# Kernel tuning notes

Measured on AMD Instinct MI355X. Metric: run time of the kernel, lower is better.

Reference implementation:

```python
import jax, jax.numpy as jnp
import numpy as np

N_NODES = 100000
N_EDGES = 1200000
IN_DIM = 64
OUT_DIM = 64


def setup_inputs() -> dict:
    key = jax.random.key(0)
    k1, k2, k3, k4, k5 = jax.random.split(key, 5)
    x = jax.random.normal(k1, (N_NODES, IN_DIM), dtype=jnp.float32)
    src = jax.random.randint(k2, (N_EDGES,), 0, N_NODES, dtype=jnp.int32)
    dst = jax.random.randint(k3, (N_EDGES,), 0, N_NODES, dtype=jnp.int32)
    # nn.Linear(in_dim, out_dim): weight [out, in], bias [out]
    bound = 1.0 / np.sqrt(IN_DIM)
    W = jax.random.uniform(k4, (OUT_DIM, IN_DIM), minval=-bound, maxval=bound, dtype=jnp.float32)
    b = jax.random.uniform(k5, (OUT_DIM,), minval=-bound, maxval=bound, dtype=jnp.float32)
    return {"x": x, "src": src, "dst": dst, "W": W, "b": b}


def reference(x, src, dst, W, b):
    # copy_u('h','m') + mean('m','h_neigh'): per-destination mean of source features
    msg_sum = jax.ops.segment_sum(x[src], dst, num_segments=N_NODES)  # [N, in_dim]
    deg = jax.ops.segment_sum(jnp.ones_like(dst, dtype=x.dtype), dst, num_segments=N_NODES)
    h = msg_sum / jnp.maximum(deg, 1.0)[:, None]  # isolated nodes -> 0 (DGL mean semantics)
    # linear: h @ W^T + b
    return h @ W.T + b
```

## Files before the change

### kernel.cpp

```cpp
#include <hip/hip_runtime.h>

#define N_NODES 100000
#define N_EDGES 1200000
#define DIM 64
#define NPW 8
#define WPB 4


__global__ __launch_bounds__(256) void hist_rank_kernel(
    const int* __restrict__ dst, int* __restrict__ counts,
    int* __restrict__ rank, int n4)
{
    int i = blockIdx.x * blockDim.x + threadIdx.x;
    if (i >= n4) return;
    int4 d = ((const int4*)dst)[i];
    int r0 = atomicAdd(&counts[d.x], 1);
    int r1 = atomicAdd(&counts[d.y], 1);
    int r2 = atomicAdd(&counts[d.z], 1);
    int r3 = atomicAdd(&counts[d.w], 1);
    ((int4*)rank)[i] = make_int4(r0, r1, r2, r3);
}

__global__ __launch_bounds__(256) void offsets_kernel(
    const int* __restrict__ counts, int* __restrict__ offsets,
    int* __restrict__ base_counter, int n)
{
    __shared__ int tmp[256];
    __shared__ int base;
    int i = blockIdx.x * 256 + threadIdx.x;
    int v = (i < n) ? counts[i] : 0;
    tmp[threadIdx.x] = v;
    __syncthreads();
    #pragma unroll
    for (int d = 1; d < 256; d <<= 1) {
        int t = (threadIdx.x >= d) ? tmp[threadIdx.x - d] : 0;
        __syncthreads();
        tmp[threadIdx.x] += t;
        __syncthreads();
    }
    if (threadIdx.x == 255) base = atomicAdd(base_counter, tmp[255]);
    __syncthreads();
    if (i < n) offsets[i] = base + tmp[threadIdx.x] - v;
}

__global__ __launch_bounds__(256) void fill_kernel(
    const int* __restrict__ src, const int* __restrict__ dst,
    const int* __restrict__ rank, const int* __restrict__ offsets,
    int* __restrict__ csr_src, int n4)
{
    int i = blockIdx.x * blockDim.x + threadIdx.x;
    if (i >= n4) return;
    int4 s = ((const int4*)src)[i];
    int4 d = ((const int4*)dst)[i];
    int4 r = ((const int4*)rank)[i];
    csr_src[offsets[d.x] + r.x] = s.x;
    csr_src[offsets[d.y] + r.y] = s.y;
    csr_src[offsets[d.z] + r.z] = s.z;
    csr_src[offsets[d.w] + r.w] = s.w;
}

__global__ __launch_bounds__(256) void aggregate_linear_kernel(
    const float* __restrict__ x, const int* __restrict__ csr_src,
    const int* __restrict__ offsets, const int* __restrict__ counts,
    const float* __restrict__ W, const float* __restrict__ bias,
    float* __restrict__ out, int n_nodes)
{
    __shared__ float Ws[DIM][68];
    __shared__ float hs[WPB][DIM];

    for (int i = threadIdx.x; i < DIM * DIM / 4; i += 256) {
        float4 wv = ((const float4*)W)[i];
        int o = (i * 4) >> 6, f = (i * 4) & 63;
        *(float4*)&Ws[o][f] = wv;
    }
    __syncthreads();

    int w    = threadIdx.x >> 6;
    int lane = threadIdx.x & 63;
    float bl = bias[lane];

    int node0 = (blockIdx.x * WPB + w) * NPW;
    #pragma unroll 1
    for (int ni = 0; ni < NPW; ++ni) {
        int node = node0 + ni;
        if (node >= n_nodes) break;

        int off = offsets[node];
        int deg = counts[node];
        int end = off + deg;
        float a0 = 0.f, a1 = 0.f, a2 = 0.f, a3 = 0.f;
        int k = off;
        for (; k + 3 < end; k += 4) {
            int s0 = csr_src[k];
            int s1 = csr_src[k + 1];
            int s2 = csr_src[k + 2];
            int s3 = csr_src[k + 3];
            a0 += x[(size_t)s0 * DIM + lane];
            a1 += x[(size_t)s1 * DIM + lane];
            a2 += x[(size_t)s2 * DIM + lane];
            a3 += x[(size_t)s3 * DIM + lane];
        }
        for (; k < end; ++k) a0 += x[(size_t)csr_src[k] * DIM + lane];
        float h = ((a0 + a1) + (a2 + a3)) / fmaxf((float)deg, 1.0f);

        hs[w][lane] = h;
        __builtin_amdgcn_wave_barrier();

        float acc = bl;
        #pragma unroll
        for (int f0 = 0; f0 < DIM; f0 += 4) {
            float4 hv = *(const float4*)&hs[w][f0];
            float4 wv = *(const float4*)&Ws[lane][f0];
            acc = fmaf(hv.x, wv.x, acc);
            acc = fmaf(hv.y, wv.y, acc);
            acc = fmaf(hv.z, wv.z, acc);
            acc = fmaf(hv.w, wv.w, acc);
        }
        out[(size_t)node * DIM + lane] = acc;
        __builtin_amdgcn_wave_barrier();
    }
}

extern "C" void kernel_launch(void* const* d_in, const int* in_sizes, int n_in,
                              void* d_out, int out_size, void* d_ws, size_t ws_size,
                              hipStream_t stream) {
    const float* x   = (const float*)d_in[0];
    const int*   src = (const int*)d_in[1];
    const int*   dst = (const int*)d_in[2];
    const float* W   = (const float*)d_in[3];
    const float* b   = (const float*)d_in[4];
    float* out = (float*)d_out;

    int* counts       = (int*)d_ws;
    int* base_counter = counts + 100032;
    int* offsets      = base_counter + 32;
    int* rank         = offsets + 100032;
    int* csr_src      = rank + N_EDGES;

    hipMemsetAsync(counts, 0, (size_t)(100032 + 32) * sizeof(int), stream);

    int n4 = N_EDGES / 4;
    int eb4 = (n4 + 255) / 256;
    int nb = (N_NODES + 255) / 256;

    hist_rank_kernel<<<eb4, 256, 0, stream>>>(dst, counts, rank, n4);
    offsets_kernel  <<<nb, 256, 0, stream>>>(counts, offsets, base_counter, N_NODES);
    fill_kernel     <<<eb4, 256, 0, stream>>>(src, dst, rank, offsets, csr_src, n4);

    int blocks = (N_NODES + WPB * NPW - 1) / (WPB * NPW);
    aggregate_linear_kernel<<<blocks, 256, 0, stream>>>(
        x, csr_src, offsets, counts, W, b, out, N_NODES);
}
```

Measured before the change: 225.2 us.

## Gather neighbor rows as float4 across quarter-waves and widen edge kernels

The aggregation loop now splits each wave into four 16-lane groups, so each group loads a whole neighbor row as float4 and eight edges are processed per iteration. Partial sums are then combined with cross-lane shuffles. The histogram and fill kernels each handle eight edges per thread, and the output store is made nontemporal. This aims to raise memory-level parallelism in the gather and cut per-edge instruction overhead, at the cost of predicated tail loads and extra shuffle reductions for low-degree nodes.

After: 214.2 us. 1.05x faster.

```diff
diff --git a/kernel.cpp b/kernel.cpp
--- a/kernel.cpp
+++ b/kernel.cpp
@@ -9,16 +9,23 @@
 
 __global__ __launch_bounds__(256) void hist_rank_kernel(
     const int* __restrict__ dst, int* __restrict__ counts,
-    int* __restrict__ rank, int n4)
+    int* __restrict__ rank, int n8)
 {
     int i = blockIdx.x * blockDim.x + threadIdx.x;
-    if (i >= n4) return;
-    int4 d = ((const int4*)dst)[i];
-    int r0 = atomicAdd(&counts[d.x], 1);
-    int r1 = atomicAdd(&counts[d.y], 1);
-    int r2 = atomicAdd(&counts[d.z], 1);
-    int r3 = atomicAdd(&counts[d.w], 1);
-    ((int4*)rank)[i] = make_int4(r0, r1, r2, r3);
+    if (i >= n8) return;
+    int4 d0 = ((const int4*)dst)[2 * i];
+    int4 d1 = ((const int4*)dst)[2 * i + 1];
+    int4 r0, r1;
+    r0.x = atomicAdd(&counts[d0.x], 1);
+    r0.y = atomicAdd(&counts[d0.y], 1);
+    r0.z = atomicAdd(&counts[d0.z], 1);
+    r0.w = atomicAdd(&counts[d0.w], 1);
+    r1.x = atomicAdd(&counts[d1.x], 1);
+    r1.y = atomicAdd(&counts[d1.y], 1);
+    r1.z = atomicAdd(&counts[d1.z], 1);
+    r1.w = atomicAdd(&counts[d1.w], 1);
+    ((int4*)rank)[2 * i]     = r0;
+    ((int4*)rank)[2 * i + 1] = r1;
 }
 
 __global__ __launch_bounds__(256) void offsets_kernel(
@@ -46,17 +53,24 @@
 __global__ __launch_bounds__(256) void fill_kernel(
     const int* __restrict__ src, const int* __restrict__ dst,
     const int* __restrict__ rank, const int* __restrict__ offsets,
-    int* __restrict__ csr_src, int n4)
+    int* __restrict__ csr_src, int n8)
 {
     int i = blockIdx.x * blockDim.x + threadIdx.x;
-    if (i >= n4) return;
-    int4 s = ((const int4*)src)[i];
-    int4 d = ((const int4*)dst)[i];
-    int4 r = ((const int4*)rank)[i];
-    csr_src[offsets[d.x] + r.x] = s.x;
-    csr_src[offsets[d.y] + r.y] = s.y;
-    csr_src[offsets[d.z] + r.z] = s.z;
-    csr_src[offsets[d.w] + r.w] = s.w;
+    if (i >= n8) return;
+    int4 s0 = ((const int4*)src)[2 * i];
+    int4 s1 = ((const int4*)src)[2 * i + 1];
+    int4 d0 = ((const int4*)dst)[2 * i];
+    int4 d1 = ((const int4*)dst)[2 * i + 1];
+    int4 r0 = ((const int4*)rank)[2 * i];
+    int4 r1 = ((const int4*)rank)[2 * i + 1];
+    csr_src[offsets[d0.x] + r0.x] = s0.x;
+    csr_src[offsets[d0.y] + r0.y] = s0.y;
+    csr_src[offsets[d0.z] + r0.z] = s0.z;
+    csr_src[offsets[d0.w] + r0.w] = s0.w;
+    csr_src[offsets[d1.x] + r1.x] = s1.x;
+    csr_src[offsets[d1.y] + r1.y] = s1.y;
+    csr_src[offsets[d1.z] + r1.z] = s1.z;
+    csr_src[offsets[d1.w] + r1.w] = s1.w;
 }
 
 __global__ __launch_bounds__(256) void aggregate_linear_kernel(
@@ -70,13 +84,15 @@
 
     for (int i = threadIdx.x; i < DIM * DIM / 4; i += 256) {
         float4 wv = ((const float4*)W)[i];
-        int o = (i * 4) >> 6, f = (i * 4) & 63;
-        *(float4*)&Ws[o][f] = wv;
+        int o = i >> 4, fq = i & 15;
+        *(float4*)&Ws[o][fq * 4] = wv;
     }
     __syncthreads();
 
     int w    = threadIdx.x >> 6;
     int lane = threadIdx.x & 63;
+    int g    = lane >> 4;
+    int gl   = lane & 15;
     float bl = bias[lane];
 
     int node0 = (blockIdx.x * WPB + w) * NPW;
@@ -88,22 +104,31 @@
         int off = offsets[node];
         int deg = counts[node];
         int end = off + deg;
-        float a0 = 0.f, a1 = 0.f, a2 = 0.f, a3 = 0.f;
-        int k = off;
-        for (; k + 3 < end; k += 4) {
-            int s0 = csr_src[k];
-            int s1 = csr_src[k + 1];
-            int s2 = csr_src[k + 2];
-            int s3 = csr_src[k + 3];
-            a0 += x[(size_t)s0 * DIM + lane];
-            a1 += x[(size_t)s1 * DIM + lane];
-            a2 += x[(size_t)s2 * DIM + lane];
-            a3 += x[(size_t)s3 * DIM + lane];
+        float4 a0 = {0.f, 0.f, 0.f, 0.f};
+        float4 a1 = {0.f, 0.f, 0.f, 0.f};
+        for (int k = off; k < end; k += 8) {
+            int e0 = k + g, e1 = k + 4 + g;
+            int s0 = csr_src[min(e0, end - 1)];
+            int s1 = csr_src[min(e1, end - 1)];
+            float4 v0 = *(const float4*)&x[(size_t)s0 * DIM + gl * 4];
+            float4 v1 = *(const float4*)&x[(size_t)s1 * DIM + gl * 4];
+            bool p0 = e0 < end, p1 = e1 < end;
+            a0.x += p0 ? v0.x : 0.f;  a0.y += p0 ? v0.y : 0.f;
+            a0.z += p0 ? v0.z : 0.f;  a0.w += p0 ? v0.w : 0.f;
+            a1.x += p1 ? v1.x : 0.f;  a1.y += p1 ? v1.y : 0.f;
+            a1.z += p1 ? v1.z : 0.f;  a1.w += p1 ? v1.w : 0.f;
         }
-        for (; k < end; ++k) a0 += x[(size_t)csr_src[k] * DIM + lane];
-        float h = ((a0 + a1) + (a2 + a3)) / fmaxf((float)deg, 1.0f);
+        a0.x += a1.x; a0.y += a1.y; a0.z += a1.z; a0.w += a1.w;
+        a0.x += __shfl_xor(a0.x, 16, 64); a0.x += __shfl_xor(a0.x, 32, 64);
+        a0.y += __shfl_xor(a0.y, 16, 64); a0.y += __shfl_xor(a0.y, 32, 64);
+        a0.z += __shfl_xor(a0.z, 16, 64); a0.z += __shfl_xor(a0.z, 32, 64);
+        a0.w += __shfl_xor(a0.w, 16, 64); a0.w += __shfl_xor(a0.w, 32, 64);
 
-        hs[w][lane] = h;
+        float inv = 1.0f / fmaxf((float)deg, 1.0f);
+        if (g == 0) {
+            float4 h4 = {a0.x * inv, a0.y * inv, a0.z * inv, a0.w * inv};
+            *(float4*)&hs[w][gl * 4] = h4;
+        }
         __builtin_amdgcn_wave_barrier();
 
         float acc = bl;
@@ -116,7 +141,7 @@
             acc = fmaf(hv.z, wv.z, acc);
             acc = fmaf(hv.w, wv.w, acc);
         }
-        out[(size_t)node * DIM + lane] = acc;
+        __builtin_nontemporal_store(acc, &out[(size_t)node * DIM + lane]);
         __builtin_amdgcn_wave_barrier();
     }
 }
@@ -139,13 +164,13 @@
 
     hipMemsetAsync(counts, 0, (size_t)(100032 + 32) * sizeof(int), stream);
 
-    int n4 = N_EDGES / 4;
-    int eb4 = (n4 + 255) / 256;
+    int n8 = N_EDGES / 8;
+    int eb8 = (n8 + 255) / 256;
     int nb = (N_NODES + 255) / 256;
 
-    hist_rank_kernel<<<eb4, 256, 0, stream>>>(dst, counts, rank, n4);
+    hist_rank_kernel<<<eb8, 256, 0, stream>>>(dst, counts, rank, n8);
     offsets_kernel  <<<nb, 256, 0, stream>>>(counts, offsets, base_counter, N_NODES);
-    fill_kernel     <<<eb4, 256, 0, stream>>>(src, dst, rank, offsets, csr_src, n4);
+    fill_kernel     <<<eb8, 256, 0, stream>>>(src, dst, rank, offsets, csr_src, n8);
 
     int blocks = (N_NODES + WPB * NPW - 1) / (WPB * NPW);
     aggregate_linear_kernel<<<blocks, 256, 0, stream>>>(
```
